# Optimization experiments

Measured on AMD Instinct MI355X. Metric: run time of the kernel, lower is better.

The kernel has to match this reference:

```python
import jax, jax.numpy as jnp
import numpy as np

B, N, C, D, O = 32, 512, 16, 256, 256


def setup_inputs() -> dict:
    key = jax.random.key(0)
    k1, k2, k3, k4, k5, k6 = jax.random.split(key, 6)
    std = 1.0 / np.sqrt(D)
    nodes = jax.random.normal(k1, (B, N, D), jnp.float32)
    children = jax.random.randint(k2, (B, N, C), 0, N)  # 0 == no-child sentinel
    w_t = jax.random.normal(k3, (D, O), jnp.float32) * std
    w_l = jax.random.normal(k4, (D, O), jnp.float32) * std
    w_r = jax.random.normal(k5, (D, O), jnp.float32) * std
    conv = jax.random.normal(k6, (O,), jnp.float32) * np.sqrt(2.0 / D)
    return {"nodes": nodes, "w_t": w_t, "w_l": w_l, "w_r": w_r, "conv": conv,
            "children": children}


def _coefs(children):
    # children: (B, N, C) int. Returns coef (B, N, C+1, 3) = stack(c_t, c_r, c_l).
    b, n, c = children.shape
    y = c + 1
    has_child = jnp.minimum(children, 1).astype(jnp.float32)          # (B,N,C)
    mask = jnp.concatenate([jnp.zeros((b, n, 1), jnp.float32), has_child], axis=2)  # (B,N,Y)
    # eta_t: 1 at slot 0 (parent), 0 elsewhere
    c_t = jnp.concatenate([jnp.ones((b, n, 1), jnp.float32),
                           jnp.zeros((b, n, c), jnp.float32)], axis=2)
    # eta_r
    ns = jnp.count_nonzero(children, axis=2).astype(jnp.float32)[..., None]  # (B,N,1)
    p = jnp.arange(-1.0, c, dtype=jnp.float32)                        # (Y,): -1,0,1,...
    child_idx = p * mask                                              # (B,N,Y)
    singles = (jnp.arange(y) == 1).astype(jnp.float32) * 0.5          # (Y,)
    denom = jnp.where(ns == 1.0, 1.0, ns - 1.0)                       # safe divide
    c_r = jnp.where(ns == 1.0,
                    jnp.broadcast_to(singles, mask.shape),
                    (1.0 - c_t) * (child_idx / denom))
    # eta_l
    c_l = (1.0 - c_t) * (1.0 - c_r) * mask
    return jnp.stack([c_t, c_r, c_l], axis=3)                         # (B,N,Y,3)


def reference(nodes, w_t, w_l, w_r, conv, children):
    b, n, d = nodes.shape
    c = children.shape[2]
    # gather children embeddings: child_emb[b,i,j] = nodes[b, children[b,i,j]]
    flat_idx = children.reshape(b, n * c)
    child_emb = jnp.take_along_axis(nodes, flat_idx[:, :, None], axis=1)
    child_emb = child_emb.reshape(b, n, c, d)
    child_emb = jnp.where((children == 0)[..., None], 0.0, child_emb)
    tree = jnp.concatenate([nodes[:, :, None, :], child_emb], axis=2)  # (B,N,Y,D)
    coef = _coefs(children)                                            # (B,N,Y,3)
    weights = jnp.stack([w_t, w_r, w_l], axis=0)                       # (3,D,O)
    agg = jnp.einsum('bnyd,bnyk->bnkd', tree, coef)                    # (B,N,3,D)
    res = jnp.einsum('bnkd,kdo->bno', agg, weights)                    # (B,N,O)
    return jax.nn.leaky_relu(res + conv, negative_slope=0.01)
```

## Files before the change

### kernel.cpp

```cpp
#include <hip/hip_runtime.h>
#include <hip/hip_bf16.h>
#include <stdint.h>

#define CC 16
#define OO 256
#define NSLAB 24
#define MT_ROWS 64
#define SLAB_ELS (MT_ROWS * 32)
#define MT_ELS (NSLAB * SLAB_ELS)
#define AGG_ELS (16384 * 768)
#define NGB 2048

typedef __attribute__((ext_vector_type(8))) short bf16x8;
typedef __attribute__((ext_vector_type(4))) float f32x4;

__device__ __forceinline__ unsigned short f2bf(float x) {
    unsigned u = __builtin_bit_cast(unsigned, x);
    u += 0x7FFFu + ((u >> 16) & 1u);
    return (unsigned short)(u >> 16);
}

__device__ __forceinline__ void st_bf4(unsigned short* p, float4 v) {
    uint2 u;
    u.x = (unsigned)f2bf(v.x) | ((unsigned)f2bf(v.y) << 16);
    u.y = (unsigned)f2bf(v.z) | ((unsigned)f2bf(v.w) << 16);
    *(uint2*)p = u;
}

__device__ __forceinline__ void cp16(const void* g, void* l) {
    __builtin_amdgcn_global_load_lds(
        (const __attribute__((address_space(1))) unsigned int*)g,
        (__attribute__((address_space(3))) unsigned int*)l, 16, 0, 0);
}

__global__ __launch_bounds__(256, 4) void gather_prep(
    const float* __restrict__ nodes, const int* __restrict__ children,
    const float* __restrict__ wt, const float* __restrict__ wrp,
    const float* __restrict__ wl, unsigned short* __restrict__ agg,
    unsigned short* __restrict__ wsb) {

    __shared__ unsigned short T[256 * 40];
    const int p = blockIdx.x;
    const int tid = threadIdx.x;

    if (p >= NGB) {
        const int slab = p - NGB;
        const int n = tid;
#pragma unroll
        for (int kk = 0; kk < 32; ++kk) {
            const int k = slab * 32 + kk;
            const float* s = (k < 256) ? wt : ((k < 512) ? wrp : wl);
            T[n * 40 + kk] = f2bf(s[(k & 255) * OO + n]);
        }
        __syncthreads();
        uint4* dst = (uint4*)(wsb + slab * 8192 + n * 32);
        const uint4* src = (const uint4*)&T[n * 40];
#pragma unroll
        for (int q = 0; q < 4; ++q) dst[q] = src[q];
        return;
    }

    const int wave = tid >> 6;
    const int lane = tid & 63;
    const int lb = (p & 7) * 256 + (p >> 3);
    const int base = lb * 8;
    const float4* g4 = (const float4*)nodes;

#pragma unroll 1
    for (int i = 0; i < 2; ++i) {
        const int nf = __builtin_amdgcn_readfirstlane(base + wave * 2 + i);
        const int brow = nf & ~511;
        const int* chp = children + (nf << 4);
        int cj[CC];
#pragma unroll
        for (int j = 0; j < CC; ++j) cj[j] = chp[j];
        int ns = 0;
#pragma unroll
        for (int j = 0; j < CC; ++j) ns += (cj[j] != 0) ? 1 : 0;
        const float inv_den = (ns > 1) ? 1.0f / (float)(ns - 1) : 0.0f;
        const bool single = (ns == 1);

        float4 pt = g4[(size_t)nf * 64 + lane];
        float4 e[CC];
#pragma unroll
        for (int j = 0; j < CC; ++j)
            e[j] = g4[(size_t)(brow + cj[j]) * 64 + lane];

        float4 ar = make_float4(0.f, 0.f, 0.f, 0.f);
        float4 al = make_float4(0.f, 0.f, 0.f, 0.f);
#pragma unroll
        for (int j = 0; j < CC; ++j) {
            const float hasf = (cj[j] != 0) ? 1.0f : 0.0f;
            const float crr_raw = single ? ((j == 0) ? 0.5f : 0.0f)
                                         : (float)j * inv_den;
            const float cr = crr_raw * hasf;
            const float cl = (1.0f - crr_raw) * hasf;
            ar.x += cr * e[j].x; ar.y += cr * e[j].y;
            ar.z += cr * e[j].z; ar.w += cr * e[j].w;
            al.x += cl * e[j].x; al.y += cl * e[j].y;
            al.z += cl * e[j].z; al.w += cl * e[j].w;
        }
        const int sl = lane >> 3;
        const int kw = (lane & 7) * 4;
        unsigned short* rowp = agg + (size_t)(nf >> 6) * MT_ELS
                                   + (size_t)(nf & 63) * 32 + kw;
        st_bf4(rowp + (size_t)(0  + sl) * SLAB_ELS, pt);
        st_bf4(rowp + (size_t)(8  + sl) * SLAB_ELS, ar);
        st_bf4(rowp + (size_t)(16 + sl) * SLAB_ELS, al);
    }
}

__global__ __launch_bounds__(256, 2) void gemm_ep(
    const unsigned short* __restrict__ agg, const unsigned short* __restrict__ wsb,
    const float* __restrict__ conv, float* __restrict__ out) {

    __shared__ unsigned short Ab[2][SLAB_ELS];
    __shared__ unsigned short Bb[2][4096];

    const int tid  = threadIdx.x;
    const int wave = tid >> 6;
    const int lane = tid & 63;
    const int quad = lane >> 4;
    const int l16  = lane & 15;
    const int mtile = blockIdx.x >> 1;
    const int ntile = blockIdx.x & 1;
    const int wrr = wave >> 1;
    const int wcc = wave & 1;

    const char* aggb = (const char*)agg + (size_t)mtile * (MT_ELS * 2);
    const char* wsbb = (const char*)wsb + ntile * 8192;
    const int toff  = tid * 16;
    const int wbase = (tid & ~63) * 16;

    f32x4 acc[2][4];
#pragma unroll
    for (int mi = 0; mi < 2; ++mi)
#pragma unroll
        for (int ni = 0; ni < 4; ++ni)
            acc[mi][ni] = (f32x4){0.f, 0.f, 0.f, 0.f};

    auto stage = [&](int s, int b) {
        const char* ga = aggb + s * 4096 + toff;
        cp16(ga, (char*)&Ab[b][0] + wbase);
        const char* gb = wsbb + s * 16384 + toff;
        cp16(gb,        (char*)&Bb[b][0] + wbase);
        cp16(gb + 4096, (char*)&Bb[b][0] + wbase + 4096);
    };

    stage(0, 0);
#pragma unroll 1
    for (int s = 0; s < NSLAB; ++s) {
        const int cur = s & 1;
        __syncthreads();
        if (s + 1 < NSLAB) stage(s + 1, cur ^ 1);

        bf16x8 af[2], bfr[4];
#pragma unroll
        for (int mi = 0; mi < 2; ++mi)
            af[mi] = *(const bf16x8*)&Ab[cur][(wrr * 32 + mi * 16 + l16) * 32 + quad * 8];
#pragma unroll
        for (int ni = 0; ni < 4; ++ni)
            bfr[ni] = *(const bf16x8*)&Bb[cur][(wcc * 64 + ni * 16 + l16) * 32 + quad * 8];
#pragma unroll
        for (int mi = 0; mi < 2; ++mi)
#pragma unroll
            for (int ni = 0; ni < 4; ++ni)
                acc[mi][ni] = __builtin_amdgcn_mfma_f32_16x16x32_bf16(
                    af[mi], bfr[ni], acc[mi][ni], 0, 0, 0);
    }

#pragma unroll
    for (int ni = 0; ni < 4; ++ni) {
        const int col = ntile * 128 + wcc * 64 + ni * 16 + l16;
        const float cv = conv[col];
#pragma unroll
        for (int mi = 0; mi < 2; ++mi) {
#pragma unroll
            for (int r = 0; r < 4; ++r) {
                const int row = mtile * 64 + wrr * 32 + mi * 16 + quad * 4 + r;
                float v = acc[mi][ni][r] + cv;
                v = (v > 0.f) ? v : 0.01f * v;
                out[(size_t)row * OO + col] = v;
            }
        }
    }
}

extern "C" void kernel_launch(void* const* d_in, const int* in_sizes, int n_in,
                              void* d_out, int out_size, void* d_ws, size_t ws_size,
                              hipStream_t stream) {
    const float* nodes    = (const float*)d_in[0];
    const float* w_t      = (const float*)d_in[1];
    const float* w_l      = (const float*)d_in[2];
    const float* w_r      = (const float*)d_in[3];
    const float* conv     = (const float*)d_in[4];
    const int*   children = (const int*)d_in[5];

    unsigned short* agg = (unsigned short*)d_ws;
    unsigned short* wsb = agg + AGG_ELS;

    gather_prep<<<NGB + 24, 256, 0, stream>>>(nodes, children, w_t, w_r, w_l,
                                              agg, wsb);
    gemm_ep<<<512, 256, 0, stream>>>(agg, wsb, conv, (float*)d_out);
}
```

Baseline: 105.2 us.

## Fuse gather-aggregation into GEMM via LDS-resident A tile with XOR swizzle

Folds the child gather and coefficient reduction into the GEMM kernel. Each 512-thread block builds its full 64x768 bf16 A tile in shared memory instead of writing an aggregated buffer to global memory and reading it back. Each block now computes all 256 output columns, so only the B weight slabs are streamed through a double buffer. The A and B layouts use an XOR swizzle to avoid LDS bank conflicts. The costs are only 256 blocks with a large LDS footprint (about 128 KB), which limits occupancy, and no overlap between the gather phase and the MFMA phase inside a block.

```diff
diff --git a/kernel.cpp b/kernel.cpp
--- a/kernel.cpp
+++ b/kernel.cpp
@@ -1,15 +1,9 @@
 #include <hip/hip_runtime.h>
-#include <hip/hip_bf16.h>
 #include <stdint.h>
 
 #define CC 16
 #define OO 256
 #define NSLAB 24
-#define MT_ROWS 64
-#define SLAB_ELS (MT_ROWS * 32)
-#define MT_ELS (NSLAB * SLAB_ELS)
-#define AGG_ELS (16384 * 768)
-#define NGB 2048
 
 typedef __attribute__((ext_vector_type(8))) short bf16x8;
 typedef __attribute__((ext_vector_type(4))) float f32x4;
@@ -20,11 +14,11 @@
     return (unsigned short)(u >> 16);
 }
 
-__device__ __forceinline__ void st_bf4(unsigned short* p, float4 v) {
+__device__ __forceinline__ uint2 pack_bf4(float4 v) {
     uint2 u;
     u.x = (unsigned)f2bf(v.x) | ((unsigned)f2bf(v.y) << 16);
     u.y = (unsigned)f2bf(v.z) | ((unsigned)f2bf(v.w) << 16);
-    *(uint2*)p = u;
+    return u;
 }
 
 __device__ __forceinline__ void cp16(const void* g, void* l) {
@@ -33,104 +27,118 @@
         (__attribute__((address_space(3))) unsigned int*)l, 16, 0, 0);
 }
 
-__global__ __launch_bounds__(256, 4) void gather_prep(
+__global__ __launch_bounds__(256) void wprep(
+    const float* __restrict__ wt, const float* __restrict__ wrp,
+    const float* __restrict__ wl, unsigned short* __restrict__ wsb) {
+
+    __shared__ __attribute__((aligned(16))) unsigned short T[256 * 40];
+    const int slab = blockIdx.x;
+    const int n = threadIdx.x;
+#pragma unroll
+    for (int kk = 0; kk < 32; ++kk) {
+        const int k = slab * 32 + kk;
+        const float* s = (k < 256) ? wt : ((k < 512) ? wrp : wl);
+        T[n * 40 + kk] = f2bf(s[(k & 255) * OO + n]);
+    }
+    __syncthreads();
+    const int f = (n >> 1) & 3;
+    uint4* dst = (uint4*)(wsb + slab * 8192 + n * 32);
+    const uint4* src = (const uint4*)&T[n * 40];
+#pragma unroll
+    for (int q = 0; q < 4; ++q) dst[q] = src[q ^ f];
+}
+
+__global__ __launch_bounds__(512, 2) void fused_gemm(
     const float* __restrict__ nodes, const int* __restrict__ children,
-    const float* __restrict__ wt, const float* __restrict__ wrp,
-    const float* __restrict__ wl, unsigned short* __restrict__ agg,
-    unsigned short* __restrict__ wsb) {
-
-    __shared__ unsigned short T[256 * 40];
-    const int p = blockIdx.x;
-    const int tid = threadIdx.x;
-
-    if (p >= NGB) {
-        const int slab = p - NGB;
-        const int n = tid;
-#pragma unroll
-        for (int kk = 0; kk < 32; ++kk) {
-            const int k = slab * 32 + kk;
-            const float* s = (k < 256) ? wt : ((k < 512) ? wrp : wl);
-            T[n * 40 + kk] = f2bf(s[(k & 255) * OO + n]);
-        }
-        __syncthreads();
-        uint4* dst = (uint4*)(wsb + slab * 8192 + n * 32);
-        const uint4* src = (const uint4*)&T[n * 40];
-#pragma unroll
-        for (int q = 0; q < 4; ++q) dst[q] = src[q];
-        return;
-    }
-
+    const unsigned short* __restrict__ wsb, const float* __restrict__ conv,
+    float* __restrict__ out) {
+
+    __shared__ __attribute__((aligned(16))) unsigned short As[NSLAB * 2048];
+    __shared__ __attribute__((aligned(16))) unsigned short Bs[2][8192];
+
+    const int tid  = threadIdx.x;
     const int wave = tid >> 6;
     const int lane = tid & 63;
-    const int lb = (p & 7) * 256 + (p >> 3);
-    const int base = lb * 8;
+    const int bid  = blockIdx.x;
+    const int mtile = ((bid & 7) << 5) | (bid >> 3);
+
+    const int toff  = tid * 16;
+    const int wbase = (tid & ~63) * 16;
+    const char* wb  = (const char*)wsb;
+
+    auto stageB = [&](int s, int b) {
+        cp16(wb + s * 16384 + toff,        (char*)&Bs[b][0] + wbase);
+        cp16(wb + s * 16384 + 8192 + toff, (char*)&Bs[b][0] + wbase + 8192);
+    };
+
+    stageB(0, 0);
+
+    const int sl    = lane >> 3;
+    const int l8    = lane & 7;
+    const int cpb   = l8 >> 1;
+    const int half8 = (lane & 1) * 8;
     const float4* g4 = (const float4*)nodes;
 
-#pragma unroll 1
-    for (int i = 0; i < 2; ++i) {
-        const int nf = __builtin_amdgcn_readfirstlane(base + wave * 2 + i);
-        const int brow = nf & ~511;
-        const int* chp = children + (nf << 4);
-        int cj[CC];
-#pragma unroll
-        for (int j = 0; j < CC; ++j) cj[j] = chp[j];
+    auto reduce_store = [&](int r, const int* cj, float4 pt, const float4* e) {
         int ns = 0;
 #pragma unroll
         for (int j = 0; j < CC; ++j) ns += (cj[j] != 0) ? 1 : 0;
         const float inv_den = (ns > 1) ? 1.0f / (float)(ns - 1) : 0.0f;
         const bool single = (ns == 1);
-
-        float4 pt = g4[(size_t)nf * 64 + lane];
-        float4 e[CC];
-#pragma unroll
-        for (int j = 0; j < CC; ++j)
-            e[j] = g4[(size_t)(brow + cj[j]) * 64 + lane];
-
         float4 ar = make_float4(0.f, 0.f, 0.f, 0.f);
         float4 al = make_float4(0.f, 0.f, 0.f, 0.f);
 #pragma unroll
         for (int j = 0; j < CC; ++j) {
             const float hasf = (cj[j] != 0) ? 1.0f : 0.0f;
-            const float crr_raw = single ? ((j == 0) ? 0.5f : 0.0f)
-                                         : (float)j * inv_den;
-            const float cr = crr_raw * hasf;
-            const float cl = (1.0f - crr_raw) * hasf;
+            const float crr  = single ? ((j == 0) ? 0.5f : 0.0f)
+                                      : (float)j * inv_den;
+            const float cr = crr * hasf;
+            const float cl = (1.0f - crr) * hasf;
             ar.x += cr * e[j].x; ar.y += cr * e[j].y;
             ar.z += cr * e[j].z; ar.w += cr * e[j].w;
             al.x += cl * e[j].x; al.y += cl * e[j].y;
             al.z += cl * e[j].z; al.w += cl * e[j].w;
         }
-        const int sl = lane >> 3;
-        const int kw = (lane & 7) * 4;
-        unsigned short* rowp = agg + (size_t)(nf >> 6) * MT_ELS
-                                   + (size_t)(nf & 63) * 32 + kw;
-        st_bf4(rowp + (size_t)(0  + sl) * SLAB_ELS, pt);
-        st_bf4(rowp + (size_t)(8  + sl) * SLAB_ELS, ar);
-        st_bf4(rowp + (size_t)(16 + sl) * SLAB_ELS, al);
-    }
-}
-
-__global__ __launch_bounds__(256, 2) void gemm_ep(
-    const unsigned short* __restrict__ agg, const unsigned short* __restrict__ wsb,
-    const float* __restrict__ conv, float* __restrict__ out) {
-
-    __shared__ unsigned short Ab[2][SLAB_ELS];
-    __shared__ unsigned short Bb[2][4096];
-
-    const int tid  = threadIdx.x;
-    const int wave = tid >> 6;
-    const int lane = tid & 63;
+        const int swz = ((cpb ^ ((r >> 1) & 3)) << 4) + half8;
+        char* rowb = (char*)As + r * 64 + swz;
+        *(uint2*)(rowb + (size_t)(0  + sl) * 4096) = pack_bf4(pt);
+        *(uint2*)(rowb + (size_t)(8  + sl) * 4096) = pack_bf4(ar);
+        *(uint2*)(rowb + (size_t)(16 + sl) * 4096) = pack_bf4(al);
+    };
+
+#pragma unroll 1
+    for (int pr = 0; pr < 4; ++pr) {
+        const int r0  = wave * 8 + pr * 2;
+        const int nf0 = __builtin_amdgcn_readfirstlane(mtile * 64 + r0);
+        const int nf1 = nf0 + 1;
+        const int brow = nf0 & ~511;
+        const int* ch0 = children + (nf0 << 4);
+        const int* ch1 = children + (nf1 << 4);
+        int cj0[CC], cj1[CC];
+#pragma unroll
+        for (int j = 0; j < CC; ++j) cj0[j] = ch0[j];
+#pragma unroll
+        for (int j = 0; j < CC; ++j) cj1[j] = ch1[j];
+
+        float4 p0 = g4[(size_t)nf0 * 64 + lane];
+        float4 p1 = g4[(size_t)nf1 * 64 + lane];
+        float4 e0[CC], e1[CC];
+#pragma unroll
+        for (int j = 0; j < CC; ++j)
+            e0[j] = g4[(size_t)(brow + cj0[j]) * 64 + lane];
+#pragma unroll
+        for (int j = 0; j < CC; ++j)
+            e1[j] = g4[(size_t)(brow + cj1[j]) * 64 + lane];
+
+        reduce_store(r0,     cj0, p0, e0);
+        reduce_store(r0 + 1, cj1, p1, e1);
+    }
+
     const int quad = lane >> 4;
     const int l16  = lane & 15;
-    const int mtile = blockIdx.x >> 1;
-    const int ntile = blockIdx.x & 1;
-    const int wrr = wave >> 1;
-    const int wcc = wave & 1;
-
-    const char* aggb = (const char*)agg + (size_t)mtile * (MT_ELS * 2);
-    const char* wsbb = (const char*)wsb + ntile * 8192;
-    const int toff  = tid * 16;
-    const int wbase = (tid & ~63) * 16;
+    const int wrr  = wave >> 2;
+    const int wcc  = wave & 3;
+    const int fx   = ((l16 >> 1) & 3) << 4;
 
     f32x4 acc[2][4];
 #pragma unroll
@@ -139,28 +147,21 @@
         for (int ni = 0; ni < 4; ++ni)
             acc[mi][ni] = (f32x4){0.f, 0.f, 0.f, 0.f};
 
-    auto stage = [&](int s, int b) {
-        const char* ga = aggb + s * 4096 + toff;
-        cp16(ga, (char*)&Ab[b][0] + wbase);
-        const char* gb = wsbb + s * 16384 + toff;
-        cp16(gb,        (char*)&Bb[b][0] + wbase);
-        cp16(gb + 4096, (char*)&Bb[b][0] + wbase + 4096);
-    };
-
-    stage(0, 0);
 #pragma unroll 1
     for (int s = 0; s < NSLAB; ++s) {
         const int cur = s & 1;
         __syncthreads();
-        if (s + 1 < NSLAB) stage(s + 1, cur ^ 1);
+        if (s + 1 < NSLAB) stageB(s + 1, cur ^ 1);
 
         bf16x8 af[2], bfr[4];
 #pragma unroll
         for (int mi = 0; mi < 2; ++mi)
-            af[mi] = *(const bf16x8*)&Ab[cur][(wrr * 32 + mi * 16 + l16) * 32 + quad * 8];
+            af[mi] = *(const bf16x8*)((const char*)As + s * 4096
+                        + (wrr * 32 + mi * 16 + l16) * 64 + (((quad << 4)) ^ fx));
 #pragma unroll
         for (int ni = 0; ni < 4; ++ni)
-            bfr[ni] = *(const bf16x8*)&Bb[cur][(wcc * 64 + ni * 16 + l16) * 32 + quad * 8];
+            bfr[ni] = *(const bf16x8*)((const char*)&Bs[cur][0]
+                        + (wcc * 64 + ni * 16 + l16) * 64 + (((quad << 4)) ^ fx));
 #pragma unroll
         for (int mi = 0; mi < 2; ++mi)
 #pragma unroll
@@ -171,7 +172,7 @@
 
 #pragma unroll
     for (int ni = 0; ni < 4; ++ni) {
-        const int col = ntile * 128 + wcc * 64 + ni * 16 + l16;
+        const int col = wcc * 64 + ni * 16 + l16;
         const float cv = conv[col];
 #pragma unroll
         for (int mi = 0; mi < 2; ++mi) {
@@ -196,10 +197,8 @@
     const float* conv     = (const float*)d_in[4];
     const int*   children = (const int*)d_in[5];
 
-    unsigned short* agg = (unsigned short*)d_ws;
-    unsigned short* wsb = agg + AGG_ELS;
-
-    gather_prep<<<NGB + 24, 256, 0, stream>>>(nodes, children, w_t, w_r, w_l,
-                                              agg, wsb);
-    gemm_ep<<<512, 256, 0, stream>>>(agg, wsb, conv, (float*)d_out);
-}
+    unsigned short* wsb = (unsigned short*)d_ws;
+
+    wprep<<<NSLAB, 256, 0, stream>>>(w_t, w_r, w_l, wsb);
+    fused_gemm<<<256, 512, 0, stream>>>(nodes, children, wsb, conv, (float*)d_out);
+}
```

After: 108.6 us. 3.3% more time.

## Widen GEMM K-slabs to 64 with XOR-swizzled LDS layout and remapped blocks

Applied to the files above, without the earlier changes.

Each GEMM K-slab grows from 32 to 64 bf16 columns, which halves the number of pipeline iterations and barriers and gives two MFMA groups per barrier. The gather and weight-prep kernels now write a 128-byte-row XOR-swizzled layout so the GEMM's LDS fragment reads avoid bank conflicts. The weight-prep path drops its LDS transpose. The GEMM block index is remapped to spread tiles across XCDs. LDS use per block doubles, which could affect occupancy, and the weight-prep reads are strided column loads.

```diff
diff --git a/kernel.cpp b/kernel.cpp
--- a/kernel.cpp
+++ b/kernel.cpp
@@ -1,14 +1,12 @@
 #include <hip/hip_runtime.h>
-#include <hip/hip_bf16.h>
 #include <stdint.h>
 
 #define CC 16
 #define OO 256
-#define NSLAB 24
-#define MT_ROWS 64
-#define SLAB_ELS (MT_ROWS * 32)
-#define MT_ELS (NSLAB * SLAB_ELS)
-#define AGG_ELS (16384 * 768)
+#define NSLAB 12
+#define SLAB_BYTES (64 * 128)
+#define MT_BYTES (NSLAB * SLAB_BYTES)
+#define AGG_BYTES (256 * MT_BYTES)
 #define NGB 2048
 
 typedef __attribute__((ext_vector_type(8))) short bf16x8;
@@ -20,11 +18,11 @@
     return (unsigned short)(u >> 16);
 }
 
-__device__ __forceinline__ void st_bf4(unsigned short* p, float4 v) {
+__device__ __forceinline__ uint2 pack_bf4(float4 v) {
     uint2 u;
     u.x = (unsigned)f2bf(v.x) | ((unsigned)f2bf(v.y) << 16);
     u.y = (unsigned)f2bf(v.z) | ((unsigned)f2bf(v.w) << 16);
-    *(uint2*)p = u;
+    return u;
 }
 
 __device__ __forceinline__ void cp16(const void* g, void* l) {
@@ -39,24 +37,31 @@
     const float* __restrict__ wl, unsigned short* __restrict__ agg,
     unsigned short* __restrict__ wsb) {
 
-    __shared__ unsigned short T[256 * 40];
     const int p = blockIdx.x;
     const int tid = threadIdx.x;
+    char* aggB = (char*)agg;
+    char* wsbB = (char*)wsb;
 
     if (p >= NGB) {
         const int slab = p - NGB;
+        const int part = slab >> 2;
+        const int k0 = (slab & 3) * 64;
+        const float* W = (part == 0) ? wt : ((part == 1) ? wrp : wl);
         const int n = tid;
-#pragma unroll
-        for (int kk = 0; kk < 32; ++kk) {
-            const int k = slab * 32 + kk;
-            const float* s = (k < 256) ? wt : ((k < 512) ? wrp : wl);
-            T[n * 40 + kk] = f2bf(s[(k & 255) * OO + n]);
-        }
-        __syncthreads();
-        uint4* dst = (uint4*)(wsb + slab * 8192 + n * 32);
-        const uint4* src = (const uint4*)&T[n * 40];
-#pragma unroll
-        for (int q = 0; q < 4; ++q) dst[q] = src[q];
+        const int f = n & 7;
+        char* dst = wsbB + slab * 32768 + n * 128;
+#pragma unroll
+        for (int q = 0; q < 8; ++q) {
+            float v[8];
+#pragma unroll
+            for (int i = 0; i < 8; ++i) v[i] = W[(k0 + q * 8 + i) * OO + n];
+            uint4 u;
+            u.x = (unsigned)f2bf(v[0]) | ((unsigned)f2bf(v[1]) << 16);
+            u.y = (unsigned)f2bf(v[2]) | ((unsigned)f2bf(v[3]) << 16);
+            u.z = (unsigned)f2bf(v[4]) | ((unsigned)f2bf(v[5]) << 16);
+            u.w = (unsigned)f2bf(v[6]) | ((unsigned)f2bf(v[7]) << 16);
+            *(uint4*)(dst + ((q ^ f) << 4)) = u;
+        }
         return;
     }
 
@@ -65,6 +70,10 @@
     const int lb = (p & 7) * 256 + (p >> 3);
     const int base = lb * 8;
     const float4* g4 = (const float4*)nodes;
+
+    const int s4  = lane >> 4;
+    const int chk = (lane & 15) >> 1;
+    const int hb  = (lane & 1) * 8;
 
 #pragma unroll 1
     for (int i = 0; i < 2; ++i) {
@@ -91,22 +100,22 @@
 #pragma unroll
         for (int j = 0; j < CC; ++j) {
             const float hasf = (cj[j] != 0) ? 1.0f : 0.0f;
-            const float crr_raw = single ? ((j == 0) ? 0.5f : 0.0f)
-                                         : (float)j * inv_den;
-            const float cr = crr_raw * hasf;
-            const float cl = (1.0f - crr_raw) * hasf;
+            const float crr  = single ? ((j == 0) ? 0.5f : 0.0f)
+                                      : (float)j * inv_den;
+            const float cr = crr * hasf;
+            const float cl = (1.0f - crr) * hasf;
             ar.x += cr * e[j].x; ar.y += cr * e[j].y;
             ar.z += cr * e[j].z; ar.w += cr * e[j].w;
             al.x += cl * e[j].x; al.y += cl * e[j].y;
             al.z += cl * e[j].z; al.w += cl * e[j].w;
         }
-        const int sl = lane >> 3;
-        const int kw = (lane & 7) * 4;
-        unsigned short* rowp = agg + (size_t)(nf >> 6) * MT_ELS
-                                   + (size_t)(nf & 63) * 32 + kw;
-        st_bf4(rowp + (size_t)(0  + sl) * SLAB_ELS, pt);
-        st_bf4(rowp + (size_t)(8  + sl) * SLAB_ELS, ar);
-        st_bf4(rowp + (size_t)(16 + sl) * SLAB_ELS, al);
+
+        const int row = nf & 63;
+        char* rowb = aggB + (size_t)(nf >> 6) * MT_BYTES + row * 128
+                   + ((chk ^ (row & 7)) << 4) + hb;
+        *(uint2*)(rowb + (size_t)(0 + s4) * SLAB_BYTES) = pack_bf4(pt);
+        *(uint2*)(rowb + (size_t)(4 + s4) * SLAB_BYTES) = pack_bf4(ar);
+        *(uint2*)(rowb + (size_t)(8 + s4) * SLAB_BYTES) = pack_bf4(al);
     }
 }
 
@@ -114,21 +123,23 @@
     const unsigned short* __restrict__ agg, const unsigned short* __restrict__ wsb,
     const float* __restrict__ conv, float* __restrict__ out) {
 
-    __shared__ unsigned short Ab[2][SLAB_ELS];
-    __shared__ unsigned short Bb[2][4096];
+    __shared__ __attribute__((aligned(16))) unsigned short Ab[2][4096];
+    __shared__ __attribute__((aligned(16))) unsigned short Bb[2][8192];
 
     const int tid  = threadIdx.x;
     const int wave = tid >> 6;
     const int lane = tid & 63;
     const int quad = lane >> 4;
     const int l16  = lane & 15;
-    const int mtile = blockIdx.x >> 1;
-    const int ntile = blockIdx.x & 1;
+    const int bid  = blockIdx.x;
+    const int lb = (bid & 7) * 64 + (bid >> 3);
+    const int mtile = lb >> 1;
+    const int ntile = lb & 1;
     const int wrr = wave >> 1;
     const int wcc = wave & 1;
 
-    const char* aggb = (const char*)agg + (size_t)mtile * (MT_ELS * 2);
-    const char* wsbb = (const char*)wsb + ntile * 8192;
+    const char* aggb = (const char*)agg + (size_t)mtile * MT_BYTES;
+    const char* wsbb = (const char*)wsb + ntile * 16384;
     const int toff  = tid * 16;
     const int wbase = (tid & ~63) * 16;
 
@@ -140,33 +151,46 @@
             acc[mi][ni] = (f32x4){0.f, 0.f, 0.f, 0.f};
 
     auto stage = [&](int s, int b) {
-        const char* ga = aggb + s * 4096 + toff;
-        cp16(ga, (char*)&Ab[b][0] + wbase);
-        const char* gb = wsbb + s * 16384 + toff;
-        cp16(gb,        (char*)&Bb[b][0] + wbase);
-        cp16(gb + 4096, (char*)&Bb[b][0] + wbase + 4096);
+        const char* ga = aggb + s * SLAB_BYTES + toff;
+        cp16(ga,        (char*)&Ab[b][0] + wbase);
+        cp16(ga + 4096, (char*)&Ab[b][0] + wbase + 4096);
+        const char* gb = wsbb + s * 32768 + toff;
+        cp16(gb,         (char*)&Bb[b][0] + wbase);
+        cp16(gb + 4096,  (char*)&Bb[b][0] + wbase + 4096);
+        cp16(gb + 8192,  (char*)&Bb[b][0] + wbase + 8192);
+        cp16(gb + 12288, (char*)&Bb[b][0] + wbase + 12288);
     };
 
     stage(0, 0);
+    const int fx = l16 & 7;
+
 #pragma unroll 1
     for (int s = 0; s < NSLAB; ++s) {
         const int cur = s & 1;
         __syncthreads();
         if (s + 1 < NSLAB) stage(s + 1, cur ^ 1);
 
-        bf16x8 af[2], bfr[4];
-#pragma unroll
-        for (int mi = 0; mi < 2; ++mi)
-            af[mi] = *(const bf16x8*)&Ab[cur][(wrr * 32 + mi * 16 + l16) * 32 + quad * 8];
-#pragma unroll
-        for (int ni = 0; ni < 4; ++ni)
-            bfr[ni] = *(const bf16x8*)&Bb[cur][(wcc * 64 + ni * 16 + l16) * 32 + quad * 8];
-#pragma unroll
-        for (int mi = 0; mi < 2; ++mi)
+        bf16x8 af[2][2], bfr[2][4];
+#pragma unroll
+        for (int h = 0; h < 2; ++h) {
+            const int co = (((h * 4 + quad) ^ fx) << 4);
+#pragma unroll
+            for (int mi = 0; mi < 2; ++mi)
+                af[h][mi] = *(const bf16x8*)((const char*)&Ab[cur][0]
+                            + (wrr * 32 + mi * 16 + l16) * 128 + co);
 #pragma unroll
             for (int ni = 0; ni < 4; ++ni)
-                acc[mi][ni] = __builtin_amdgcn_mfma_f32_16x16x32_bf16(
-                    af[mi], bfr[ni], acc[mi][ni], 0, 0, 0);
+                bfr[h][ni] = *(const bf16x8*)((const char*)&Bb[cur][0]
+                            + (wcc * 64 + ni * 16 + l16) * 128 + co);
+        }
+#pragma unroll
+        for (int h = 0; h < 2; ++h)
+#pragma unroll
+            for (int mi = 0; mi < 2; ++mi)
+#pragma unroll
+                for (int ni = 0; ni < 4; ++ni)
+                    acc[mi][ni] = __builtin_amdgcn_mfma_f32_16x16x32_bf16(
+                        af[h][mi], bfr[h][ni], acc[mi][ni], 0, 0, 0);
     }
 
 #pragma unroll
@@ -197,9 +221,9 @@
     const int*   children = (const int*)d_in[5];
 
     unsigned short* agg = (unsigned short*)d_ws;
-    unsigned short* wsb = agg + AGG_ELS;
-
-    gather_prep<<<NGB + 24, 256, 0, stream>>>(nodes, children, w_t, w_r, w_l,
-                                              agg, wsb);
+    unsigned short* wsb = (unsigned short*)((char*)d_ws + AGG_BYTES);
+
+    gather_prep<<<NGB + NSLAB, 256, 0, stream>>>(nodes, children, w_t, w_r, w_l,
+                                                 agg, wsb);
     gemm_ep<<<512, 256, 0, stream>>>(agg, wsb, conv, (float*)d_out);
 }
```

New measurement: 105.0 us. Within noise of the previous version (-0.2%).
